# Kernel tuning notes

Hardware: AMD Instinct MI355X
Metric: run time of the kernel (lower is better)

## Reference

```python
import jax, jax.numpy as jnp
import numpy as np

B, CL, H, W, NP = 128, 8, 16, 16, 32   # batch, primary cap length, height, width, n primary capsules
NC, CLO, ITER = 10, 16, 3              # n output capsules, output capsule length, routing iterations


def squash(t):
    # TensorMONK Activations 'squash': squash along axis 2 of a 3D tensor
    ss = jnp.sum(t * t, axis=2, keepdims=True)
    return (ss / (1.0 + ss)) * t / jnp.sqrt(ss)


def setup_inputs() -> dict:
    key = jax.random.key(0)
    k1, k2 = jax.random.split(key)
    tensor = jax.random.normal(k1, (B, CL, H, W, NP), dtype=jnp.float32)
    # nn.Parameter(torch.randn(...).normal_(0.0, 0.1)) -> N(0, 0.1)
    weight = 0.1 * jax.random.normal(k2, (CL * H * W, NP, NC * CLO), dtype=jnp.float32)
    return {"tensor": tensor, "weight": weight}


def reference(tensor, weight):
    b, cl, h, w, n_prim = tensor.shape
    # flatten spatial/length dims, squash along primary-capsule axis (dim 2, faithful to source)
    x = squash(tensor.reshape(b, -1, n_prim))                  # (B, P, N) with P = cl*h*w
    # (B,P,1,N) @ (P,N,K) broadcasted matmul -> (B,P,K)
    u = jnp.einsum('bpn,pnk->bpk', x, weight)
    u = u.reshape(b, cl, h, w, NC, CLO)                        # (B, cl, h, w, NC, CLO)
    bias = jnp.zeros((b, cl, h, w, NC), dtype=tensor.dtype)
    v = None
    for i in range(ITER):  # fixed small iteration count
        c = jax.nn.softmax(bias, axis=4)                       # softmax over output capsules
        s = jnp.einsum('bchwn,bchwnk->bnk', c, u)              # weighted sum over cl,h,w
        v = squash(s)                                          # squash along capsule length (axis 2)
        if i < ITER - 1:
            bias = bias + jnp.einsum('bchwnk,bnk->bchwn', u, v)
    return v
```

## Files before the change

kernel.cpp:

```cpp
#include <hip/hip_runtime.h>
#include <cstdint>

typedef unsigned short u16;
typedef __attribute__((ext_vector_type(8))) short bf16x8;
typedef __attribute__((ext_vector_type(4))) float f32x4;

#define B_   128
#define P_   2048
#define NC_  10
#define F_   160
#define NBLK 512
#define PPB  4
#define NTHR 512

__device__ __forceinline__ u16 f2bf(float f) {
    union { float f; unsigned u; } v; v.f = f;
    unsigned r = v.u + 0x7FFFu + ((v.u >> 16) & 1u);
    return (u16)(r >> 16);
}
__device__ __forceinline__ float bf2f(u16 h) {
    union { unsigned u; float f; } v; v.u = ((unsigned)h) << 16;
    return v.f;
}

__device__ __forceinline__ void gl_lds16(const void* g, void* l) {
    typedef __attribute__((address_space(3))) unsigned lds_uint;
    typedef __attribute__((address_space(1))) const unsigned glob_uint;
    __builtin_amdgcn_global_load_lds((glob_uint*)(uintptr_t)g,
                                     (lds_uint*)(unsigned)(uintptr_t)l, 16, 0, 0);
}

__global__ void k_prep(const float* __restrict__ t, const float* __restrict__ w,
                       u16* __restrict__ xb, u16* __restrict__ wb) {
    const int blk = blockIdx.x, tid = threadIdx.x;
    if (blk < 4096) {
        int g = blk * 256 + tid;
        int pair = g >> 2, sub = g & 3;
        int p = pair & 2047, b = pair >> 11;
        const float4* tg = (const float4*)t;
        int fi = pair * 8 + sub * 2;
        float4 va = tg[fi], vb = tg[fi + 1];
        float ss = va.x*va.x + va.y*va.y + va.z*va.z + va.w*va.w
                 + vb.x*vb.x + vb.y*vb.y + vb.z*vb.z + vb.w*vb.w;
        ss += __shfl_xor(ss, 1);
        ss += __shfl_xor(ss, 2);
        float fct = ss / ((1.f + ss) * sqrtf(ss));
        u16 h[8] __attribute__((aligned(16)));
        h[0]=f2bf(va.x*fct); h[1]=f2bf(va.y*fct); h[2]=f2bf(va.z*fct); h[3]=f2bf(va.w*fct);
        h[4]=f2bf(vb.x*fct); h[5]=f2bf(vb.y*fct); h[6]=f2bf(vb.z*fct); h[7]=f2bf(vb.w*fct);
        int off = (sub + (b >> 1)) & 3;
        *(uint4*)(xb + p * 4096 + b * 32 + off * 8) = *(const uint4*)h;
    } else {
        __shared__ u16 wl[32 * F_];
        int p = blk - 4096;
        const float4* wp = (const float4*)(w + p * 32 * F_);
        for (int e4 = tid; e4 < 1280; e4 += 256) {
            float4 v = wp[e4];
            u16 h[4] __attribute__((aligned(8)));
            h[0]=f2bf(v.x); h[1]=f2bf(v.y); h[2]=f2bf(v.z); h[3]=f2bf(v.w);
            *(ushort4*)(wl + e4 * 4) = *(const ushort4*)h;
        }
        __syncthreads();
        u16* wo = wb + p * 5120;
        for (int sid = tid; sid < 640; sid += 256) {
            int f = sid >> 2, k0 = (sid & 3) << 3, q = sid & 3;
            u16 tmp[8] __attribute__((aligned(16)));
#pragma unroll
            for (int j = 0; j < 8; ++j) tmp[j] = wl[(k0 + j) * F_ + f];
            int off = (q + (f >> 1)) & 3;
            *(uint4*)(wo + f * 32 + off * 8) = *(const uint4*)tmp;
        }
    }
}

template<int MODE>
__global__ __launch_bounds__(NTHR, 2) void k_pass(
        const u16* __restrict__ xb, const u16* __restrict__ wb,
        const float* __restrict__ vprev, u16* __restrict__ s_part)
{
    __shared__ __align__(16) u16 xt[2][4096];
    __shared__ __align__(16) u16 wt[2][5120];
    const int tid = threadIdx.x, blk = blockIdx.x;
    const int L = tid & 63, wv = tid >> 6;
    const int q = L >> 4, col = L & 15;
    const int b = wv * 16 + col;
    const int p0 = blk * PPB;
    const int off8 = ((q + (col >> 1)) & 3) * 8;

    float4 vv[NC_];
    if (MODE != 0) {
#pragma unroll
        for (int n = 0; n < NC_; ++n)
            vv[n] = *(const float4*)(vprev + b * F_ + n * 16 + q * 4);
    }

    f32x4 s_acc[NC_];
#pragma unroll
    for (int n = 0; n < NC_; ++n) s_acc[n] = (f32x4){0.f, 0.f, 0.f, 0.f};

    auto issue = [&](int p, int c) {
        const u16* xg = xb + p * 4096 + wv * 512 + L * 8;
        const u16* wg = wb + p * 5120 + wv * 512 + L * 8;
        gl_lds16(xg, &xt[c][wv * 512]);
        gl_lds16(wg, &wt[c][wv * 512]);
        if (wv < 2)
            gl_lds16(wb + p * 5120 + (8 + wv) * 512 + L * 8, &wt[c][(8 + wv) * 512]);
    };

    issue(p0, 0);
#pragma unroll
    for (int pp = 0; pp < PPB; ++pp) {
        __builtin_amdgcn_s_waitcnt(0x0f70);
        __syncthreads();
        if (pp + 1 < PPB) issue(p0 + pp + 1, (pp + 1) & 1);
        const u16* xc = xt[pp & 1];
        const u16* wc = wt[pp & 1];

        bf16x8 bfrag = *(const bf16x8*)&xc[b * 32 + off8];
        if (MODE == 0) {
#pragma unroll
            for (int n = 0; n < NC_; ++n) {
                bf16x8 afrag = *(const bf16x8*)&wc[(n * 16 + col) * 32 + off8];
                s_acc[n] = __builtin_amdgcn_mfma_f32_16x16x32_bf16(afrag, bfrag, s_acc[n], 0, 0, 0);
            }
        } else {
            float tt[NC_];
#pragma unroll
            for (int n = 0; n < NC_; ++n) {
                bf16x8 afrag = *(const bf16x8*)&wc[(n * 16 + col) * 32 + off8];
                f32x4 z = {0.f, 0.f, 0.f, 0.f};
                f32x4 acc = __builtin_amdgcn_mfma_f32_16x16x32_bf16(afrag, bfrag, z, 0, 0, 0);
                float t = acc[0]*vv[n].x + acc[1]*vv[n].y + acc[2]*vv[n].z + acc[3]*vv[n].w;
                t += __shfl_xor(t, 16);
                t += __shfl_xor(t, 32);
                tt[n] = t;
            }
            float mx = tt[0];
#pragma unroll
            for (int n = 1; n < NC_; ++n) mx = fmaxf(mx, tt[n]);
            float den = 0.f;
#pragma unroll
            for (int n = 0; n < NC_; ++n) { tt[n] = __expf(tt[n] - mx); den += tt[n]; }
            float inv = 1.f / den;
#pragma unroll
            for (int n = 0; n < NC_; ++n) {
                bf16x8 afrag = *(const bf16x8*)&wc[(n * 16 + col) * 32 + off8];
                f32x4 z = {0.f, 0.f, 0.f, 0.f};
                f32x4 acc = __builtin_amdgcn_mfma_f32_16x16x32_bf16(afrag, bfrag, z, 0, 0, 0);
                float cf = tt[n] * inv;
#pragma unroll
                for (int r = 0; r < 4; ++r) s_acc[n][r] += cf * acc[r];
            }
        }
    }

    u16* sp = s_part + blk * (B_ * F_);
    const float sc = (MODE == 0) ? 0.1f : 1.f;
#pragma unroll
    for (int n = 0; n < NC_; ++n) {
        u16 h[4] __attribute__((aligned(8)));
#pragma unroll
        for (int r = 0; r < 4; ++r) h[r] = f2bf(s_acc[n][r] * sc);
        *(ushort4*)(sp + b * F_ + n * 16 + q * 4) = *(const ushort4*)h;
    }
}

template<int ADD>
__global__ void k_red(const u16* __restrict__ s_part,
                      const float* __restrict__ vprev, float* __restrict__ vout) {
    __shared__ float r0s[256], r1s[256];
    const int tid = threadIdx.x, blk = blockIdx.x;
    const int pid = tid & 31, part = tid >> 5;
    const uint* sp = (const uint*)s_part;
    const int opair = blk * 32 + pid;
    float a0 = 0.f, a1 = 0.f;
#pragma unroll 8
    for (int g = part; g < NBLK; g += 8) {
        uint u = sp[g * 10240 + opair];
        a0 += bf2f((u16)(u & 0xffff));
        a1 += bf2f((u16)(u >> 16));
    }
    r0s[tid] = a0; r1s[tid] = a1;
    __syncthreads();
    if (tid < 32) {
        float s0 = 0.f, s1 = 0.f;
#pragma unroll
        for (int k = 0; k < 8; ++k) { s0 += r0s[k * 32 + tid]; s1 += r1s[k * 32 + tid]; }
        float sq = s0 * s0 + s1 * s1;
        sq += __shfl_xor(sq, 1);
        sq += __shfl_xor(sq, 2);
        sq += __shfl_xor(sq, 4);
        float fct = sq / ((1.f + sq) * sqrtf(sq));
        float2 o = make_float2(s0 * fct, s1 * fct);
        if (ADD) {
            float2 pv = *(const float2*)(vprev + 2 * (blk * 32 + tid));
            o.x += pv.x; o.y += pv.y;
        }
        *(float2*)(vout + 2 * (blk * 32 + tid)) = o;
    }
}

extern "C" void kernel_launch(void* const* d_in, const int* in_sizes, int n_in,
                              void* d_out, int out_size, void* d_ws, size_t ws_size,
                              hipStream_t stream) {
    const float* tensor = (const float*)d_in[0];
    const float* weight = (const float*)d_in[1];
    float* out = (float*)d_out;
    char* ws = (char*)d_ws;

    u16*   xb     = (u16*)(ws);
    u16*   wb     = (u16*)(ws + 16777216);
    u16*   s_part = (u16*)(ws + 37748736);
    float* v0     = (float*)(ws + 58720256);
    float* vs     = (float*)(ws + 58802176);

    k_prep<<<6144, 256, 0, stream>>>(tensor, weight, xb, wb);

    k_pass<0><<<NBLK, NTHR, 0, stream>>>(xb, wb, nullptr, s_part);
    k_red<0><<<320, 256, 0, stream>>>(s_part, nullptr, v0);
    k_pass<1><<<NBLK, NTHR, 0, stream>>>(xb, wb, v0, s_part);
    k_red<1><<<320, 256, 0, stream>>>(s_part, v0, vs);
    k_pass<2><<<NBLK, NTHR, 0, stream>>>(xb, wb, vs, s_part);
    k_red<0><<<320, 256, 0, stream>>>(s_part, nullptr, out);
}
```

Baseline: 176.8 us.

## Prefetch all tiles upfront, stage partial-sum stores through LDS, pad prep transpose

Issues global-to-LDS loads for all four p-tiles at kernel start into separate LDS buffers and waits on them incrementally with per-tile vmcnt counts, replacing the double-buffered loop. The output partial sums are written to LDS first, then copied out with coalesced 16-byte stores. The weight transpose in the prep kernel uses a padded row stride to reduce LDS bank conflicts. This increases LDS usage per block, which could limit occupancy.

After: 179.0 us. About the same (+1.2%).

```diff
diff --git a/kernel.cpp b/kernel.cpp
--- a/kernel.cpp
+++ b/kernel.cpp
@@ -12,6 +12,7 @@
 #define NBLK 512
 #define PPB  4
 #define NTHR 512
+#define WLS  162
 
 __device__ __forceinline__ u16 f2bf(float f) {
     union { float f; unsigned u; } v; v.f = f;
@@ -51,14 +52,15 @@
         int off = (sub + (b >> 1)) & 3;
         *(uint4*)(xb + p * 4096 + b * 32 + off * 8) = *(const uint4*)h;
     } else {
-        __shared__ u16 wl[32 * F_];
+        __shared__ u16 wl[32 * WLS];
         int p = blk - 4096;
         const float4* wp = (const float4*)(w + p * 32 * F_);
         for (int e4 = tid; e4 < 1280; e4 += 256) {
             float4 v = wp[e4];
+            int k = e4 / 40, fg = e4 % 40;
             u16 h[4] __attribute__((aligned(8)));
             h[0]=f2bf(v.x); h[1]=f2bf(v.y); h[2]=f2bf(v.z); h[3]=f2bf(v.w);
-            *(ushort4*)(wl + e4 * 4) = *(const ushort4*)h;
+            *(ushort4*)(wl + k * WLS + fg * 4) = *(const ushort4*)h;
         }
         __syncthreads();
         u16* wo = wb + p * 5120;
@@ -66,9 +68,57 @@
             int f = sid >> 2, k0 = (sid & 3) << 3, q = sid & 3;
             u16 tmp[8] __attribute__((aligned(16)));
 #pragma unroll
-            for (int j = 0; j < 8; ++j) tmp[j] = wl[(k0 + j) * F_ + f];
+            for (int j = 0; j < 8; ++j) tmp[j] = wl[(k0 + j) * WLS + f];
             int off = (q + (f >> 1)) & 3;
             *(uint4*)(wo + f * 32 + off * 8) = *(const uint4*)tmp;
+        }
+    }
+}
+
+template<int PP, int MODE>
+__device__ __forceinline__ void tile_step(
+    const u16* __restrict__ xt, const u16* __restrict__ wt,
+    f32x4 (&s_acc)[NC_], const float4 (&vv)[NC_],
+    int wv, int b, int col, int off8)
+{
+    if (wv < 2) __builtin_amdgcn_s_waitcnt(0x0f70 | (3 * (3 - PP)));
+    else        __builtin_amdgcn_s_waitcnt(0x0f70 | (2 * (3 - PP)));
+    __builtin_amdgcn_s_barrier();
+
+    bf16x8 bfrag = *(const bf16x8*)&xt[b * 32 + off8];
+    if (MODE == 0) {
+#pragma unroll
+        for (int n = 0; n < NC_; ++n) {
+            bf16x8 afrag = *(const bf16x8*)&wt[(n * 16 + col) * 32 + off8];
+            s_acc[n] = __builtin_amdgcn_mfma_f32_16x16x32_bf16(afrag, bfrag, s_acc[n], 0, 0, 0);
+        }
+    } else {
+        float tt[NC_];
+#pragma unroll
+        for (int n = 0; n < NC_; ++n) {
+            bf16x8 afrag = *(const bf16x8*)&wt[(n * 16 + col) * 32 + off8];
+            f32x4 z = {0.f, 0.f, 0.f, 0.f};
+            f32x4 acc = __builtin_amdgcn_mfma_f32_16x16x32_bf16(afrag, bfrag, z, 0, 0, 0);
+            float t = acc[0]*vv[n].x + acc[1]*vv[n].y + acc[2]*vv[n].z + acc[3]*vv[n].w;
+            t += __shfl_xor(t, 16);
+            t += __shfl_xor(t, 32);
+            tt[n] = t;
+        }
+        float mx = tt[0];
+#pragma unroll
+        for (int n = 1; n < NC_; ++n) mx = fmaxf(mx, tt[n]);
+        float den = 0.f;
+#pragma unroll
+        for (int n = 0; n < NC_; ++n) { tt[n] = __expf(tt[n] - mx); den += tt[n]; }
+        float inv = 1.f / den;
+#pragma unroll
+        for (int n = 0; n < NC_; ++n) {
+            bf16x8 afrag = *(const bf16x8*)&wt[(n * 16 + col) * 32 + off8];
+            f32x4 z = {0.f, 0.f, 0.f, 0.f};
+            f32x4 acc = __builtin_amdgcn_mfma_f32_16x16x32_bf16(afrag, bfrag, z, 0, 0, 0);
+            float cf = tt[n] * inv;
+#pragma unroll
+            for (int r = 0; r < 4; ++r) s_acc[n][r] += cf * acc[r];
         }
     }
 }
@@ -78,8 +128,8 @@
         const u16* __restrict__ xb, const u16* __restrict__ wb,
         const float* __restrict__ vprev, u16* __restrict__ s_part)
 {
-    __shared__ __align__(16) u16 xt[2][4096];
-    __shared__ __align__(16) u16 wt[2][5120];
+    __shared__ __align__(16) u16 xt[PPB][4096];
+    __shared__ __align__(16) u16 wt[PPB][5120];
     const int tid = threadIdx.x, blk = blockIdx.x;
     const int L = tid & 63, wv = tid >> 6;
     const int q = L >> 4, col = L & 15;
@@ -94,75 +144,40 @@
             vv[n] = *(const float4*)(vprev + b * F_ + n * 16 + q * 4);
     }
 
+#pragma unroll
+    for (int t = 0; t < PPB; ++t) {
+        int p = p0 + t;
+        gl_lds16(xb + p * 4096 + wv * 512 + L * 8, &xt[t][wv * 512]);
+        gl_lds16(wb + p * 5120 + wv * 512 + L * 8, &wt[t][wv * 512]);
+        if (wv < 2)
+            gl_lds16(wb + p * 5120 + (8 + wv) * 512 + L * 8, &wt[t][(8 + wv) * 512]);
+    }
+
     f32x4 s_acc[NC_];
 #pragma unroll
     for (int n = 0; n < NC_; ++n) s_acc[n] = (f32x4){0.f, 0.f, 0.f, 0.f};
 
-    auto issue = [&](int p, int c) {
-        const u16* xg = xb + p * 4096 + wv * 512 + L * 8;
-        const u16* wg = wb + p * 5120 + wv * 512 + L * 8;
-        gl_lds16(xg, &xt[c][wv * 512]);
-        gl_lds16(wg, &wt[c][wv * 512]);
-        if (wv < 2)
-            gl_lds16(wb + p * 5120 + (8 + wv) * 512 + L * 8, &wt[c][(8 + wv) * 512]);
-    };
-
-    issue(p0, 0);
-#pragma unroll
-    for (int pp = 0; pp < PPB; ++pp) {
-        __builtin_amdgcn_s_waitcnt(0x0f70);
-        __syncthreads();
-        if (pp + 1 < PPB) issue(p0 + pp + 1, (pp + 1) & 1);
-        const u16* xc = xt[pp & 1];
-        const u16* wc = wt[pp & 1];
-
-        bf16x8 bfrag = *(const bf16x8*)&xc[b * 32 + off8];
-        if (MODE == 0) {
-#pragma unroll
-            for (int n = 0; n < NC_; ++n) {
-                bf16x8 afrag = *(const bf16x8*)&wc[(n * 16 + col) * 32 + off8];
-                s_acc[n] = __builtin_amdgcn_mfma_f32_16x16x32_bf16(afrag, bfrag, s_acc[n], 0, 0, 0);
-            }
-        } else {
-            float tt[NC_];
-#pragma unroll
-            for (int n = 0; n < NC_; ++n) {
-                bf16x8 afrag = *(const bf16x8*)&wc[(n * 16 + col) * 32 + off8];
-                f32x4 z = {0.f, 0.f, 0.f, 0.f};
-                f32x4 acc = __builtin_amdgcn_mfma_f32_16x16x32_bf16(afrag, bfrag, z, 0, 0, 0);
-                float t = acc[0]*vv[n].x + acc[1]*vv[n].y + acc[2]*vv[n].z + acc[3]*vv[n].w;
-                t += __shfl_xor(t, 16);
-                t += __shfl_xor(t, 32);
-                tt[n] = t;
-            }
-            float mx = tt[0];
-#pragma unroll
-            for (int n = 1; n < NC_; ++n) mx = fmaxf(mx, tt[n]);
-            float den = 0.f;
-#pragma unroll
-            for (int n = 0; n < NC_; ++n) { tt[n] = __expf(tt[n] - mx); den += tt[n]; }
-            float inv = 1.f / den;
-#pragma unroll
-            for (int n = 0; n < NC_; ++n) {
-                bf16x8 afrag = *(const bf16x8*)&wc[(n * 16 + col) * 32 + off8];
-                f32x4 z = {0.f, 0.f, 0.f, 0.f};
-                f32x4 acc = __builtin_amdgcn_mfma_f32_16x16x32_bf16(afrag, bfrag, z, 0, 0, 0);
-                float cf = tt[n] * inv;
-#pragma unroll
-                for (int r = 0; r < 4; ++r) s_acc[n][r] += cf * acc[r];
-            }
-        }
-    }
-
-    u16* sp = s_part + blk * (B_ * F_);
+    tile_step<0, MODE>(xt[0], wt[0], s_acc, vv, wv, b, col, off8);
+    tile_step<1, MODE>(xt[1], wt[1], s_acc, vv, wv, b, col, off8);
+    tile_step<2, MODE>(xt[2], wt[2], s_acc, vv, wv, b, col, off8);
+    tile_step<3, MODE>(xt[3], wt[3], s_acc, vv, wv, b, col, off8);
+
+    __syncthreads();
+    u16* ls = &wt[0][0];
     const float sc = (MODE == 0) ? 0.1f : 1.f;
 #pragma unroll
     for (int n = 0; n < NC_; ++n) {
         u16 h[4] __attribute__((aligned(8)));
 #pragma unroll
         for (int r = 0; r < 4; ++r) h[r] = f2bf(s_acc[n][r] * sc);
-        *(ushort4*)(sp + b * F_ + n * 16 + q * 4) = *(const ushort4*)h;
-    }
+        *(ushort4*)&ls[b * F_ + n * 16 + q * 4] = *(const ushort4*)h;
+    }
+    __syncthreads();
+    const uint4* lsv = (const uint4*)ls;
+    uint4* gp = (uint4*)(s_part + blk * (B_ * F_));
+#pragma unroll
+    for (int i = 0; i < 5; ++i)
+        gp[i * 512 + tid] = lsv[i * 512 + tid];
 }
 
 template<int ADD>
```
